# Performance work log

Hardware: AMD Instinct MI355X
Metric: run time of the kernel (lower is better)

## Reference

```python
import jax, jax.numpy as jnp
import numpy as np

B, N, D, H = 8, 1024, 1024, 16
DK = D // H


def setup_inputs() -> dict:
    key = jax.random.key(0)
    ks = jax.random.split(key, 5)
    s_in = 1.0 / np.sqrt(D)
    return {
        "x": jax.random.normal(ks[0], (B, N, D), dtype=jnp.float32),
        "w_qkv": jax.random.uniform(ks[1], (D, 3 * D), jnp.float32, -s_in, s_in),
        "b_qkv": jax.random.uniform(ks[2], (3 * D,), jnp.float32, -s_in, s_in),
        "w_proj": jax.random.uniform(ks[3], (D, D), jnp.float32, -s_in, s_in),
        "b_proj": jax.random.uniform(ks[4], (D,), jnp.float32, -s_in, s_in),
    }


def reference(x, w_qkv, b_qkv, w_proj, b_proj):
    # x: (B, N, D)
    qkv = x @ w_qkv + b_qkv                      # (B, N, 3D)
    q, k, v = jnp.split(qkv, 3, axis=-1)
    # reshape to (B, H, N, DK)
    def heads(t):
        return t.reshape(B, N, H, DK).transpose(0, 2, 1, 3)
    q, k, v = heads(q), heads(k), heads(v)
    scale = 1.0 / np.sqrt(DK).astype(np.float32)
    scores = jnp.einsum("bhnd,bhmd->bhnm", q, k) * scale  # (B, H, N, N)
    attn = jax.nn.softmax(scores, axis=-1)
    out = jnp.einsum("bhnm,bhmd->bhnd", attn, v)          # (B, H, N, DK)
    out = out.transpose(0, 2, 1, 3).reshape(B, N, D)
    return out @ w_proj + b_proj
```

## Files before the change

kernel.cpp:

```cpp
#include <hip/hip_runtime.h>
#include <hip/hip_bf16.h>


#define BB 8
#define NN 1024
#define DD 1024
#define HH 16
#define DK 64
#define TOK (BB * NN)
#define QKVN (3 * DD)

typedef __attribute__((ext_vector_type(8))) short bf16x8;
typedef __attribute__((ext_vector_type(4))) float f32x4;
typedef __attribute__((ext_vector_type(4))) short short4v;
typedef __attribute__((ext_vector_type(4))) float float4v;

static __device__ __forceinline__ short f2bf(float f) {
  union { float f; unsigned u; } v; v.f = f;
  unsigned r = (v.u + 0x7FFFu + ((v.u >> 16) & 1u)) >> 16;
  return (short)r;
}
static __device__ __forceinline__ short f2bf_rn(float f) {
  __hip_bfloat16 h(f);
  short s;
  __builtin_memcpy(&s, &h, 2);
  return s;
}
static __device__ __forceinline__ float fexp2(float x) {
#if __has_builtin(__builtin_amdgcn_exp2f)
  return __builtin_amdgcn_exp2f(x);
#else
  return __expf(x * 0.69314718056f);
#endif
}

static __device__ __forceinline__ void gload_lds16(const short* g, short* lds, int lane) {
#if __has_builtin(__builtin_amdgcn_global_load_lds)
  __builtin_amdgcn_global_load_lds((const __attribute__((address_space(1))) void*)g,
                                   (__attribute__((address_space(3))) void*)lds, 16, 0, 0);
#else
  ((bf16x8*)lds)[lane] = *(const bf16x8*)g;
#endif
}

static __device__ __forceinline__ void block_barrier() {
  asm volatile("" ::: "memory");
  __builtin_amdgcn_s_barrier();
  asm volatile("" ::: "memory");
}

__global__ __launch_bounds__(256) void cast_f32_bf16(const float* __restrict__ in,
                                                     short* __restrict__ out, long n) {
  long i = ((long)blockIdx.x * blockDim.x + threadIdx.x) * 4;
  if (i >= n) return;
  float4v v = *(const float4v*)(in + i);
  short4v o;
  o[0] = f2bf(v[0]); o[1] = f2bf(v[1]); o[2] = f2bf(v[2]); o[3] = f2bf(v[3]);
  *(short4v*)(out + i) = o;
}

__global__ __launch_bounds__(256) void transpose_cast(const float* __restrict__ in,
                                                      short* __restrict__ out,
                                                      int rows, int cols) {
  __shared__ float tile[32][33];
  int bx = blockIdx.x * 32;
  int by = blockIdx.y * 32;
  int tx = threadIdx.x, ty = threadIdx.y;
#pragma unroll
  for (int q = 0; q < 4; q++)
    tile[ty + 8 * q][tx] = in[(long)(by + ty + 8 * q) * cols + bx + tx];
  __syncthreads();
#pragma unroll
  for (int q = 0; q < 4; q++)
    out[(long)(bx + ty + 8 * q) * rows + by + tx] = f2bf(tile[tx][ty + 8 * q]);
}

__global__ __launch_bounds__(512, 2) void gemm256(const short* __restrict__ A,
                                                  const short* __restrict__ Bt,
                                                  const float* __restrict__ bias,
                                                  short* __restrict__ Cqk,
                                                  int M, int N, int K, int ldc) {
  __shared__ __align__(16) short lds[2][2][2][128 * 64];
  const int tid = threadIdx.x;
  const int wid = tid >> 6, lane = tid & 63;
  const int r = lane & 15, g = lane >> 4;
  const int wm = wid >> 2, wn = wid & 3;

  const int nwg = gridDim.x * gridDim.y;
  const int flat = blockIdx.y * gridDim.x + blockIdx.x;
  const int swz = (flat & 7) * (nwg >> 3) + (flat >> 3);
  const int bx = swz % gridDim.x, by = swz / gridDim.x;
  const long tileM = (long)by * 256, tileN = (long)bx * 256;

  f32x4 acc[8][4] = {};

  const int sc = ((lane & 7) ^ ((lane >> 3) & 7)) * 8;
  const int srl = lane >> 3;

  const int akc0 = ((0 + g) ^ (r & 7)) * 8;
  const int akc1 = ((4 + g) ^ (r & 7)) * 8;
  const int bn0 = (wn & 1) * 64;
  const int bhh = wn >> 1;

#define STAGEA(buf, h, Tt)                                                          \
  {                                                                                 \
    _Pragma("unroll") for (int j = 0; j < 2; j++)                                   \
      gload_lds16(A + (tileM + (h) * 128 + wid * 16 + j * 8 + srl) * (long)K +      \
                      (Tt) * 64 + sc,                                               \
                  &lds[buf][0][h][(wid * 2 + j) * 512], lane);                      \
  }
#define STAGEB(buf, h, Tt)                                                          \
  {                                                                                 \
    _Pragma("unroll") for (int j = 0; j < 2; j++)                                   \
      gload_lds16(Bt + (tileN + (h) * 128 + wid * 16 + j * 8 + srl) * (long)K +     \
                      (Tt) * 64 + sc,                                               \
                  &lds[buf][1][h][(wid * 2 + j) * 512], lane);                      \
  }
#define READ_A(q, p)                                                                \
  af[0][0] = *(const bf16x8*)&lds[q][0][wm][((p) * 32 + r) * 64 + akc0];            \
  af[0][1] = *(const bf16x8*)&lds[q][0][wm][((p) * 32 + r) * 64 + akc1];            \
  af[1][0] = *(const bf16x8*)&lds[q][0][wm][((p) * 32 + 16 + r) * 64 + akc0];       \
  af[1][1] = *(const bf16x8*)&lds[q][0][wm][((p) * 32 + 16 + r) * 64 + akc1];
#define READ_B(q)                                                                   \
  {                                                                                 \
    const short* Bh = &lds[q][1][bhh][0];                                           \
    _Pragma("unroll") for (int fn = 0; fn < 4; fn++) {                              \
      bf[fn][0] = *(const bf16x8*)&Bh[(bn0 + fn * 16 + r) * 64 + akc0];             \
      bf[fn][1] = *(const bf16x8*)&Bh[(bn0 + fn * 16 + r) * 64 + akc1];             \
    }                                                                               \
  }
#define WAITL()                                                                     \
  asm volatile("s_waitcnt lgkmcnt(0)" ::: "memory");                                \
  __builtin_amdgcn_sched_barrier(0);
#define MFMA_P(p)                                                                   \
  __builtin_amdgcn_s_setprio(1);                                                    \
  _Pragma("unroll") for (int fmi = 0; fmi < 2; fmi++)                               \
      _Pragma("unroll") for (int fn = 0; fn < 4; fn++) {                            \
    acc[2 * (p) + fmi][fn] = __builtin_amdgcn_mfma_f32_16x16x32_bf16(               \
        af[fmi][0], bf[fn][0], acc[2 * (p) + fmi][fn], 0, 0, 0);                    \
    acc[2 * (p) + fmi][fn] = __builtin_amdgcn_mfma_f32_16x16x32_bf16(               \
        af[fmi][1], bf[fn][1], acc[2 * (p) + fmi][fn], 0, 0, 0);                    \
  }                                                                                 \
  __builtin_amdgcn_s_setprio(0);

  const int NT = K >> 6;
  const int NIT = NT >> 1;

  STAGEA(0, 0, 0); STAGEA(0, 1, 0); STAGEB(0, 0, 0); STAGEB(0, 1, 0);
  STAGEB(1, 0, 1); STAGEB(1, 1, 1);
  asm volatile("s_waitcnt vmcnt(4)" ::: "memory");
  block_barrier();

  for (int i = 0; i < NIT; ++i) {
    const int t1 = 2 * i + 1, t2 = 2 * i + 2, t3 = 2 * i + 3;
    const bool full = (i < NIT - 1);
    bf16x8 af[2][2], bf[4][2];

    READ_A(0, 0); READ_B(0);
    STAGEA(1, 0, t1);
    block_barrier(); WAITL(); MFMA_P(0); block_barrier();

    READ_A(0, 1);
    STAGEA(1, 1, t1);
    block_barrier(); WAITL(); MFMA_P(1); block_barrier();

    READ_A(0, 2);
    if (full) STAGEB(0, 0, t2);
    block_barrier(); WAITL(); MFMA_P(2); block_barrier();

    READ_A(0, 3);
    if (full) STAGEB(0, 1, t2);
    if (full) asm volatile("s_waitcnt vmcnt(4)" ::: "memory");
    else      asm volatile("s_waitcnt vmcnt(0)" ::: "memory");
    block_barrier(); WAITL(); MFMA_P(3); block_barrier();

    READ_A(1, 0); READ_B(1);
    if (full) STAGEA(0, 0, t2);
    block_barrier(); WAITL(); MFMA_P(0); block_barrier();

    READ_A(1, 1);
    if (full) STAGEA(0, 1, t2);
    block_barrier(); WAITL(); MFMA_P(1); block_barrier();

    READ_A(1, 2);
    if (full) STAGEB(1, 0, t3);
    block_barrier(); WAITL(); MFMA_P(2); block_barrier();

    READ_A(1, 3);
    if (full) STAGEB(1, 1, t3);
    if (full) asm volatile("s_waitcnt vmcnt(4)" ::: "memory");
    block_barrier(); WAITL(); MFMA_P(3); block_barrier();
  }
#undef STAGEA
#undef STAGEB
#undef READ_A
#undef READ_B
#undef WAITL
#undef MFMA_P

#pragma unroll
  for (int fm = 0; fm < 8; fm++) {
    long rowb = tileM + wm * 128 + fm * 16 + g * 4;
#pragma unroll
    for (int fn = 0; fn < 4; fn++) {
      long cn = tileN + wn * 64 + fn * 16 + r;
      float bv = bias[cn];
      Cqk[(rowb + 0) * ldc + cn] = f2bf(acc[fm][fn][0] + bv);
      Cqk[(rowb + 1) * ldc + cn] = f2bf(acc[fm][fn][1] + bv);
      Cqk[(rowb + 2) * ldc + cn] = f2bf(acc[fm][fn][2] + bv);
      Cqk[(rowb + 3) * ldc + cn] = f2bf(acc[fm][fn][3] + bv);
    }
  }
}

template <int MODE>
__global__ __launch_bounds__(256) void gemm_bt(const short* __restrict__ A,
                                               const short* __restrict__ Bt,
                                               const float* __restrict__ bias,
                                               void* __restrict__ Cout,
                                               short* __restrict__ vT,
                                               int M, int N, int K, int ldc) {
  __shared__ __align__(16) short As[2][128 * 32];
  __shared__ __align__(16) short Bs[2][128 * 32];
  const int tid = threadIdx.x;
  const int w = tid >> 6, lane = tid & 63;
  const int r = lane & 15, g = lane >> 4;
  const int wm = w >> 1, wn = w & 1;

  const int nwg = gridDim.x * gridDim.y;
  const int flat = blockIdx.y * gridDim.x + blockIdx.x;
  const int swz = (flat & 7) * (nwg >> 3) + (flat >> 3);
  const int bx = swz % gridDim.x, by = swz / gridDim.x;

  const long tileM = (long)by * 128;
  const long tileN = (long)bx * 128;

  f32x4 acc[4][4] = {};

  const int rowInChunk = lane >> 2;
  const int colOff = ((lane & 3) ^ ((lane >> 3) & 3)) * 8;
  const int rdChunk = (g ^ ((r >> 1) & 3)) * 8;

  const int nt = K >> 5;
#pragma unroll
  for (int issue = 0; issue < 2; ++issue) {
    int c = w * 2 + issue;
    gload_lds16(A + (tileM + c * 16 + rowInChunk) * (long)K + colOff, &As[0][c * 512], lane);
    gload_lds16(Bt + (tileN + c * 16 + rowInChunk) * (long)K + colOff, &Bs[0][c * 512], lane);
  }
  __syncthreads();

  for (int t = 0; t < nt; ++t) {
    const int cur = t & 1;
    if (t + 1 < nt) {
      const int k0 = (t + 1) << 5;
#pragma unroll
      for (int issue = 0; issue < 2; ++issue) {
        int c = w * 2 + issue;
        gload_lds16(A + (tileM + c * 16 + rowInChunk) * (long)K + k0 + colOff,
                    &As[cur ^ 1][c * 512], lane);
        gload_lds16(Bt + (tileN + c * 16 + rowInChunk) * (long)K + k0 + colOff,
                    &Bs[cur ^ 1][c * 512], lane);
      }
    }

    bf16x8 a[4], b[4];
#pragma unroll
    for (int i = 0; i < 4; i++)
      a[i] = *(const bf16x8*)&As[cur][(wm * 64 + i * 16 + r) * 32 + rdChunk];
#pragma unroll
    for (int i = 0; i < 4; i++)
      b[i] = *(const bf16x8*)&Bs[cur][(wn * 64 + i * 16 + r) * 32 + rdChunk];
#pragma unroll
    for (int i = 0; i < 4; i++)
#pragma unroll
      for (int ii = 0; ii < 4; ii++)
        acc[i][ii] = __builtin_amdgcn_mfma_f32_16x16x32_bf16(a[i], b[ii], acc[i][ii], 0, 0, 0);

    __syncthreads();
  }

#pragma unroll
  for (int i = 0; i < 4; i++) {
    long rowb = tileM + wm * 64 + i * 16 + g * 4;
#pragma unroll
    for (int ii = 0; ii < 4; ii++) {
      long cn = tileN + wn * 64 + ii * 16 + r;
      float bv = bias[cn];
      float v0 = acc[i][ii][0] + bv;
      float v1 = acc[i][ii][1] + bv;
      float v2 = acc[i][ii][2] + bv;
      float v3 = acc[i][ii][3] + bv;
      if constexpr (MODE == 0) {
        float* C = (float*)Cout;
        C[(rowb + 0) * ldc + cn] = v0;
        C[(rowb + 1) * ldc + cn] = v1;
        C[(rowb + 2) * ldc + cn] = v2;
        C[(rowb + 3) * ldc + cn] = v3;
      } else {
        int hc = (int)cn;
        int b = (int)(rowb >> 10);
        int n0 = (int)(rowb & 1023);
        int pos = (n0 & ~31) + 8 * ((n0 >> 2) & 3) + 4 * ((n0 >> 4) & 1);
        long va = ((long)(b * 16 + (hc >> 6)) * 64 + (hc & 63)) * 1024 + pos;
        short4v sv;
        sv[0] = f2bf(v0); sv[1] = f2bf(v1); sv[2] = f2bf(v2); sv[3] = f2bf(v3);
        *(short4v*)&vT[va] = sv;
      }
    }
  }
}

__global__ __launch_bounds__(512) void attn_kernel(const short* __restrict__ qk,
                                                   const short* __restrict__ vT,
                                                   short* __restrict__ attn_out) {
  __shared__ __align__(16) short Ks[64 * 64];
  __shared__ __align__(16) short Vs[64 * 64];

  const int nwg = gridDim.x * gridDim.y;
  const int flat = blockIdx.y * gridDim.x + blockIdx.x;
  const int swz = (flat & 7) * (nwg >> 3) + (flat >> 3);
  const int bh = swz >> 2;
  const int qt = swz & 3;

  const int bb = bh >> 4, h = bh & 15;
  const int tid = threadIdx.x;
  const int wid = tid >> 6, lane = tid & 63;
  const int r = lane & 15, g = lane >> 4;
  const int qbase = qt * 256 + wid * 32;
  const int RS = 2048;
  const long base = (long)bb * NN * RS;
  const short* Qp = qk + base + h * 64;
  const short* Kp = qk + base + DD + h * 64;
  const short* vTh = vT + (long)bh * 64 * 1024;

  const int srow = 8 * wid + (lane >> 3);
  const int sj = (lane & 7) ^ (lane >> 3);

  bf16x8 qf[2][2];
#pragma unroll
  for (int qg = 0; qg < 2; qg++) {
    const short* qrow = Qp + (long)(qbase + 16 * qg + r) * RS;
    qf[qg][0] = *(const bf16x8*)(qrow + 8 * g);
    qf[qg][1] = *(const bf16x8*)(qrow + 32 + 8 * g);
  }

  const float C = 0.18033688f;
  float lsum[2] = {0.0f, 0.0f};
  f32x4 o[2][4] = {};

  for (int kv0 = 0; kv0 < NN; kv0 += 64) {
    __syncthreads();
    gload_lds16(Kp + (long)(kv0 + srow) * RS + sj * 8, &Ks[wid * 512], lane);
    gload_lds16(vTh + (long)srow * 1024 + kv0 + sj * 8, &Vs[wid * 512], lane);
    __syncthreads();

    bf16x8 kf[2][2][2];
#pragma unroll
    for (int c = 0; c < 2; c++)
#pragma unroll
      for (int u = 0; u < 2; u++) {
        int krow = 32 * c + 16 * u + r;
#pragma unroll
        for (int s = 0; s < 2; s++)
          kf[c][u][s] = *(const bf16x8*)&Ks[krow * 64 + (((4 * s + g) ^ (r & 7)) * 8)];
      }

    bf16x8 pf[2][2];
#pragma unroll
    for (int qg = 0; qg < 2; qg++) {
      f32x4 s[2][2];
      __builtin_amdgcn_s_setprio(1);
#pragma unroll
      for (int c = 0; c < 2; c++)
#pragma unroll
        for (int u = 0; u < 2; u++) {
          f32x4 t = {};
          t = __builtin_amdgcn_mfma_f32_16x16x32_bf16(kf[c][u][0], qf[qg][0], t, 0, 0, 0);
          s[c][u] = __builtin_amdgcn_mfma_f32_16x16x32_bf16(kf[c][u][1], qf[qg][1], t, 0, 0, 0);
        }
      __builtin_amdgcn_s_setprio(0);

      float pv[16];
#pragma unroll
      for (int c = 0; c < 2; c++)
#pragma unroll
        for (int j = 0; j < 4; j++) {
          pv[8 * c + j] = fexp2(s[c][0][j] * C);
          pv[8 * c + 4 + j] = fexp2(s[c][1][j] * C);
        }

      float s8[8];
#pragma unroll
      for (int j = 0; j < 8; j++) s8[j] = pv[j] + pv[j + 8];
#pragma unroll
      for (int j = 0; j < 4; j++) s8[j] = s8[j] + s8[j + 4];
      float ps = (s8[0] + s8[1]) + (s8[2] + s8[3]);
      ps += __shfl_xor(ps, 16);
      ps += __shfl_xor(ps, 32);
      lsum[qg] += ps;
#pragma unroll
      for (int c = 0; c < 2; c++)
#pragma unroll
        for (int j = 0; j < 8; j++) pf[qg][c][j] = f2bf_rn(pv[8 * c + j]);
    }

#pragma unroll
    for (int t = 0; t < 4; t++) {
      int vrow = 16 * t + r;
#pragma unroll
      for (int c = 0; c < 2; c++) {
        bf16x8 vt = *(const bf16x8*)&Vs[vrow * 64 + (((4 * c + g) ^ (r & 7)) * 8)];
        __builtin_amdgcn_s_setprio(1);
        o[0][t] = __builtin_amdgcn_mfma_f32_16x16x32_bf16(vt, pf[0][c], o[0][t], 0, 0, 0);
        o[1][t] = __builtin_amdgcn_mfma_f32_16x16x32_bf16(vt, pf[1][c], o[1][t], 0, 0, 0);
        __builtin_amdgcn_s_setprio(0);
      }
    }
  }

#pragma unroll
  for (int qg = 0; qg < 2; qg++) {
    float inv = 1.0f / lsum[qg];
    long orow = (long)(bb * NN + qbase + 16 * qg + r) * DD + h * 64;
#pragma unroll
    for (int t = 0; t < 4; t++) {
      short4v svv;
#pragma unroll
      for (int j = 0; j < 4; j++) svv[j] = f2bf(o[qg][t][j] * inv);
      *(short4v*)&attn_out[orow + 16 * t + 4 * g] = svv;
    }
  }
}

extern "C" void kernel_launch(void* const* d_in, const int* in_sizes, int n_in,
                              void* d_out, int out_size, void* d_ws, size_t ws_size,
                              hipStream_t stream) {
  const float* x = (const float*)d_in[0];
  const float* w_qkv = (const float*)d_in[1];
  const float* b_qkv = (const float*)d_in[2];
  const float* w_proj = (const float*)d_in[3];
  const float* b_proj = (const float*)d_in[4];
  float* out = (float*)d_out;

  short* ws = (short*)d_ws;
  short* xb = ws;
  short* wqkvT = xb + (long)TOK * DD;
  short* wprojT = wqkvT + (long)QKVN * DD;
  short* qkb = wprojT + (long)DD * DD;
  short* vT = qkb + (long)TOK * 2048;
  short* attn = vT + (long)TOK * DD;

  cast_f32_bf16<<<(TOK * DD) / (256 * 4), 256, 0, stream>>>(x, xb, (long)TOK * DD);
  transpose_cast<<<dim3(QKVN / 32, DD / 32), dim3(32, 8), 0, stream>>>(w_qkv, wqkvT, DD, QKVN);
  transpose_cast<<<dim3(DD / 32, DD / 32), dim3(32, 8), 0, stream>>>(w_proj, wprojT, DD, DD);

  gemm256<<<dim3(2048 / 256, TOK / 256), 512, 0, stream>>>(xb, wqkvT, b_qkv, qkb,
                                                           TOK, 2048, DD, 2048);

  gemm_bt<2><<<dim3(DD / 128, TOK / 128), 256, 0, stream>>>(
      xb, wqkvT + (long)2048 * DD, b_qkv + 2048, nullptr, vT, TOK, DD, DD, 0);

  attn_kernel<<<dim3(4, BB * HH), 512, 0, stream>>>(qkb, vT, attn);

  gemm_bt<0><<<dim3(DD / 128, TOK / 128), 256, 0, stream>>>(attn, wprojT, b_proj, out, nullptr,
                                                            TOK, DD, DD, DD);
}
```

Baseline: 154.2 us.

## Merge prep casts into one launch and double attention KV tile to 128

Folds the x cast and the two weight transpose-casts into a single prep kernel that dispatches on block index, removing two kernel launches. The attention kernel now stages 128 keys/values per iteration instead of 64, with a new XOR swizzle for the wider V tile. This halves the number of barrier pairs per KV sweep. The cost is doubled LDS use per block and a larger unrolled inner loop, which may raise register pressure.

Result: slower. 158.4 us (+2.7%).

```diff
diff --git a/kernel.cpp b/kernel.cpp
--- a/kernel.cpp
+++ b/kernel.cpp
@@ -49,23 +49,34 @@
   asm volatile("" ::: "memory");
 }
 
-__global__ __launch_bounds__(256) void cast_f32_bf16(const float* __restrict__ in,
-                                                     short* __restrict__ out, long n) {
-  long i = ((long)blockIdx.x * blockDim.x + threadIdx.x) * 4;
-  if (i >= n) return;
-  float4v v = *(const float4v*)(in + i);
-  short4v o;
-  o[0] = f2bf(v[0]); o[1] = f2bf(v[1]); o[2] = f2bf(v[2]); o[3] = f2bf(v[3]);
-  *(short4v*)(out + i) = o;
-}
-
-__global__ __launch_bounds__(256) void transpose_cast(const float* __restrict__ in,
-                                                      short* __restrict__ out,
-                                                      int rows, int cols) {
+__global__ __launch_bounds__(256) void prep(const float* __restrict__ x,
+                                            short* __restrict__ xb,
+                                            const float* __restrict__ wq,
+                                            short* __restrict__ wqT,
+                                            const float* __restrict__ wp,
+                                            short* __restrict__ wpT) {
   __shared__ float tile[32][33];
-  int bx = blockIdx.x * 32;
-  int by = blockIdx.y * 32;
-  int tx = threadIdx.x, ty = threadIdx.y;
+  int bid = blockIdx.x;
+  const int tid = threadIdx.x;
+  if (bid < 8192) {
+    long i = ((long)bid * 256 + tid) * 4;
+    float4v v = *(const float4v*)(x + i);
+    short4v o2;
+    o2[0] = f2bf(v[0]); o2[1] = f2bf(v[1]); o2[2] = f2bf(v[2]); o2[3] = f2bf(v[3]);
+    *(short4v*)(xb + i) = o2;
+    return;
+  }
+  bid -= 8192;
+  const float* in; short* out; int rows, cols, bx, by;
+  if (bid < 3072) {
+    in = wq; out = wqT; rows = 1024; cols = 3072;
+    bx = (bid % 96) * 32; by = (bid / 96) * 32;
+  } else {
+    bid -= 3072;
+    in = wp; out = wpT; rows = 1024; cols = 1024;
+    bx = (bid & 31) * 32; by = (bid >> 5) * 32;
+  }
+  int tx = tid & 31, ty = tid >> 5;
 #pragma unroll
   for (int q = 0; q < 4; q++)
     tile[ty + 8 * q][tx] = in[(long)(by + ty + 8 * q) * cols + bx + tx];
@@ -314,8 +325,8 @@
 __global__ __launch_bounds__(512) void attn_kernel(const short* __restrict__ qk,
                                                    const short* __restrict__ vT,
                                                    short* __restrict__ attn_out) {
-  __shared__ __align__(16) short Ks[64 * 64];
-  __shared__ __align__(16) short Vs[64 * 64];
+  __shared__ __align__(16) short Ks[128 * 64];
+  __shared__ __align__(16) short Vs[64 * 128];
 
   const int nwg = gridDim.x * gridDim.y;
   const int flat = blockIdx.y * gridDim.x + blockIdx.x;
@@ -334,8 +345,10 @@
   const short* Kp = qk + base + DD + h * 64;
   const short* vTh = vT + (long)bh * 64 * 1024;
 
-  const int srow = 8 * wid + (lane >> 3);
-  const int sj = (lane & 7) ^ (lane >> 3);
+  const int skrow = lane >> 3;
+  const int skj = (lane & 7) ^ skrow;
+  const int svrow = lane >> 4;
+  const int svc = lane & 15;
 
   bf16x8 qf[2][2];
 #pragma unroll
@@ -349,72 +362,82 @@
   float lsum[2] = {0.0f, 0.0f};
   f32x4 o[2][4] = {};
 
-  for (int kv0 = 0; kv0 < NN; kv0 += 64) {
+  for (int kv0 = 0; kv0 < NN; kv0 += 128) {
     __syncthreads();
-    gload_lds16(Kp + (long)(kv0 + srow) * RS + sj * 8, &Ks[wid * 512], lane);
-    gload_lds16(vTh + (long)srow * 1024 + kv0 + sj * 8, &Vs[wid * 512], lane);
+#pragma unroll
+    for (int j = 0; j < 2; j++) {
+      int krow = wid * 16 + j * 8 + skrow;
+      gload_lds16(Kp + (long)(kv0 + krow) * RS + skj * 8, &Ks[(wid * 16 + j * 8) * 64], lane);
+      int vrow = wid * 8 + j * 4 + svrow;
+      int sc2 = svc ^ (vrow & 15);
+      gload_lds16(vTh + (long)vrow * 1024 + kv0 + sc2 * 8, &Vs[(wid * 8 + j * 4) * 128], lane);
+    }
     __syncthreads();
 
-    bf16x8 kf[2][2][2];
-#pragma unroll
-    for (int c = 0; c < 2; c++)
-#pragma unroll
-      for (int u = 0; u < 2; u++) {
-        int krow = 32 * c + 16 * u + r;
-#pragma unroll
-        for (int s = 0; s < 2; s++)
-          kf[c][u][s] = *(const bf16x8*)&Ks[krow * 64 + (((4 * s + g) ^ (r & 7)) * 8)];
+#pragma unroll
+    for (int hh = 0; hh < 2; hh++) {
+      bf16x8 kf[2][2][2];
+#pragma unroll
+      for (int c = 0; c < 2; c++)
+#pragma unroll
+        for (int u = 0; u < 2; u++) {
+          int krow = 64 * hh + 32 * c + 16 * u + r;
+#pragma unroll
+          for (int s = 0; s < 2; s++)
+            kf[c][u][s] = *(const bf16x8*)&Ks[krow * 64 + (((4 * s + g) ^ (r & 7)) * 8)];
+        }
+
+      bf16x8 pf[2][2];
+#pragma unroll
+      for (int qg = 0; qg < 2; qg++) {
+        f32x4 s[2][2];
+        __builtin_amdgcn_s_setprio(1);
+#pragma unroll
+        for (int c = 0; c < 2; c++)
+#pragma unroll
+          for (int u = 0; u < 2; u++) {
+            f32x4 t = {};
+            t = __builtin_amdgcn_mfma_f32_16x16x32_bf16(kf[c][u][0], qf[qg][0], t, 0, 0, 0);
+            s[c][u] = __builtin_amdgcn_mfma_f32_16x16x32_bf16(kf[c][u][1], qf[qg][1], t, 0, 0, 0);
+          }
+        __builtin_amdgcn_s_setprio(0);
+
+        float pv[16];
+#pragma unroll
+        for (int c = 0; c < 2; c++)
+#pragma unroll
+          for (int j = 0; j < 4; j++) {
+            pv[8 * c + j] = fexp2(s[c][0][j] * C);
+            pv[8 * c + 4 + j] = fexp2(s[c][1][j] * C);
+          }
+
+        float s8[8];
+#pragma unroll
+        for (int j = 0; j < 8; j++) s8[j] = pv[j] + pv[j + 8];
+#pragma unroll
+        for (int j = 0; j < 4; j++) s8[j] = s8[j] + s8[j + 4];
+        float ps = (s8[0] + s8[1]) + (s8[2] + s8[3]);
+        ps += __shfl_xor(ps, 16);
+        ps += __shfl_xor(ps, 32);
+        lsum[qg] += ps;
+#pragma unroll
+        for (int c = 0; c < 2; c++)
+#pragma unroll
+          for (int j = 0; j < 8; j++) pf[qg][c][j] = f2bf_rn(pv[8 * c + j]);
       }
 
-    bf16x8 pf[2][2];
-#pragma unroll
-    for (int qg = 0; qg < 2; qg++) {
-      f32x4 s[2][2];
-      __builtin_amdgcn_s_setprio(1);
-#pragma unroll
-      for (int c = 0; c < 2; c++)
-#pragma unroll
-        for (int u = 0; u < 2; u++) {
-          f32x4 t = {};
-          t = __builtin_amdgcn_mfma_f32_16x16x32_bf16(kf[c][u][0], qf[qg][0], t, 0, 0, 0);
-          s[c][u] = __builtin_amdgcn_mfma_f32_16x16x32_bf16(kf[c][u][1], qf[qg][1], t, 0, 0, 0);
+#pragma unroll
+      for (int t = 0; t < 4; t++) {
+        int vrow = 16 * t + r;
+#pragma unroll
+        for (int c = 0; c < 2; c++) {
+          int slot = ((2 * hh + c) * 4 + g) ^ r;
+          bf16x8 vt = *(const bf16x8*)&Vs[vrow * 128 + slot * 8];
+          __builtin_amdgcn_s_setprio(1);
+          o[0][t] = __builtin_amdgcn_mfma_f32_16x16x32_bf16(vt, pf[0][c], o[0][t], 0, 0, 0);
+          o[1][t] = __builtin_amdgcn_mfma_f32_16x16x32_bf16(vt, pf[1][c], o[1][t], 0, 0, 0);
+          __builtin_amdgcn_s_setprio(0);
         }
-      __builtin_amdgcn_s_setprio(0);
-
-      float pv[16];
-#pragma unroll
-      for (int c = 0; c < 2; c++)
-#pragma unroll
-        for (int j = 0; j < 4; j++) {
-          pv[8 * c + j] = fexp2(s[c][0][j] * C);
-          pv[8 * c + 4 + j] = fexp2(s[c][1][j] * C);
-        }
-
-      float s8[8];
-#pragma unroll
-      for (int j = 0; j < 8; j++) s8[j] = pv[j] + pv[j + 8];
-#pragma unroll
-      for (int j = 0; j < 4; j++) s8[j] = s8[j] + s8[j + 4];
-      float ps = (s8[0] + s8[1]) + (s8[2] + s8[3]);
-      ps += __shfl_xor(ps, 16);
-      ps += __shfl_xor(ps, 32);
-      lsum[qg] += ps;
-#pragma unroll
-      for (int c = 0; c < 2; c++)
-#pragma unroll
-        for (int j = 0; j < 8; j++) pf[qg][c][j] = f2bf_rn(pv[8 * c + j]);
-    }
-
-#pragma unroll
-    for (int t = 0; t < 4; t++) {
-      int vrow = 16 * t + r;
-#pragma unroll
-      for (int c = 0; c < 2; c++) {
-        bf16x8 vt = *(const bf16x8*)&Vs[vrow * 64 + (((4 * c + g) ^ (r & 7)) * 8)];
-        __builtin_amdgcn_s_setprio(1);
-        o[0][t] = __builtin_amdgcn_mfma_f32_16x16x32_bf16(vt, pf[0][c], o[0][t], 0, 0, 0);
-        o[1][t] = __builtin_amdgcn_mfma_f32_16x16x32_bf16(vt, pf[1][c], o[1][t], 0, 0, 0);
-        __builtin_amdgcn_s_setprio(0);
       }
     }
   }
@@ -451,9 +474,7 @@
   short* vT = qkb + (long)TOK * 2048;
   short* attn = vT + (long)TOK * DD;
 
-  cast_f32_bf16<<<(TOK * DD) / (256 * 4), 256, 0, stream>>>(x, xb, (long)TOK * DD);
-  transpose_cast<<<dim3(QKVN / 32, DD / 32), dim3(32, 8), 0, stream>>>(w_qkv, wqkvT, DD, QKVN);
-  transpose_cast<<<dim3(DD / 32, DD / 32), dim3(32, 8), 0, stream>>>(w_proj, wprojT, DD, DD);
+  prep<<<8192 + 3072 + 1024, 256, 0, stream>>>(x, xb, w_qkv, wqkvT, w_proj, wprojT);
 
   gemm256<<<dim3(2048 / 256, TOK / 256), 512, 0, stream>>>(xb, wqkvT, b_qkv, qkb,
                                                            TOK, 2048, DD, 2048);
```
